# Optimization experiments

Hardware: AMD Instinct MI355X
Metric: run time of the kernel (lower is better)

## Reference

```python
import jax, jax.numpy as jnp
import numpy as np

HEADS = 16
DIM_HEAD = 64
MAX_FREQ = 256.0  # lucidrains RotaryEmbedding(freqs_for='pixel', max_freq=256)


def axial_freqs(H, W, dim_head):
    # per-axis rotary dim = dim_head // 2 (RotaryEmbedding(dim=head_dim//2))
    d = dim_head // 2
    base = jnp.linspace(1.0, MAX_FREQ / 2.0, d // 2) * jnp.pi  # (d/2,)

    def axis(n):
        pos = jnp.linspace(-1.0, 1.0, n)              # pixel positions
        f = pos[:, None] * base                        # (n, d/2)
        return jnp.repeat(f, 2, axis=-1)               # (n, d) interleaved pairs

    fh = jnp.broadcast_to(axis(H)[:, None, :], (H, W, d))
    fw = jnp.broadcast_to(axis(W)[None, :, :], (H, W, d))
    return jnp.concatenate([fh, fw], axis=-1)          # (H, W, dim_head)


def apply_rope(t, freqs):
    # t: (B,T,H,W,h,d); freqs: (H,W,d)
    f = freqs[:, :, None, :]                           # broadcast over heads
    x = t.reshape(t.shape[:-1] + (t.shape[-1] // 2, 2))
    x1, x2 = x[..., 0], x[..., 1]
    rot = jnp.stack([-x2, x1], axis=-1).reshape(t.shape)  # rotate_half (interleaved)
    return t * jnp.cos(f) + rot * jnp.sin(f)


def setup_inputs() -> dict:
    key = jax.random.key(0)
    k1, k2, k3 = jax.random.split(key, 3)
    B, T, H, W, D = 1, 8, 32, 32, 1024
    inner = HEADS * DIM_HEAD
    x = jax.random.normal(k1, (B, T, H, W, D), dtype=jnp.float32)
    Wqkv = jax.random.normal(k2, (D, 3 * inner), dtype=jnp.float32) * 0.02
    Wout = jax.random.normal(k3, (inner, D), dtype=jnp.float32) * 0.02
    bout = jnp.zeros((D,), dtype=jnp.float32)
    return {"x": x, "Wqkv": Wqkv, "Wout": Wout, "bout": bout}


def reference(x, Wqkv, Wout, bout):
    B, T, H, W, D = x.shape
    qkv = x @ Wqkv                                     # (B,T,H,W,3*inner)
    q, k, v = jnp.split(qkv, 3, axis=-1)
    shp = (B, T, H, W, HEADS, DIM_HEAD)
    q, k, v = q.reshape(shp), k.reshape(shp), v.reshape(shp)
    freqs = axial_freqs(H, W, DIM_HEAD)
    q = apply_rope(q, freqs)
    k = apply_rope(k, freqs)
    S = H * W
    q = q.reshape(B * T, S, HEADS, DIM_HEAD)
    k = k.reshape(B * T, S, HEADS, DIM_HEAD)
    v = v.reshape(B * T, S, HEADS, DIM_HEAD)
    scale = 1.0 / np.sqrt(DIM_HEAD).astype(np.float32)
    att = jnp.einsum('bshd,bthd->bhst', q, k) * scale  # (BT, h, S, S)
    att = jax.nn.softmax(att, axis=-1)
    o = jnp.einsum('bhst,bthd->bshd', att, v)          # (BT, S, h, d)
    o = o.reshape(B, T, H, W, HEADS * DIM_HEAD)
    return o @ Wout + bout
```

## Files before the change

### kernel.cpp

```cpp
#include <hip/hip_runtime.h>
#include <math.h>

#define DMODEL 1024
#define NQKV   3072
#define SEQ    1024
#define NH     16
#define DH     64
#define HS     (SEQ*DH)
constexpr float PI_F   = 3.14159265358979323846f;
constexpr float LOG2E  = 1.44269504088896f;

typedef _Float16 half8   __attribute__((ext_vector_type(8)));
typedef _Float16 half4   __attribute__((ext_vector_type(4)));
typedef float    floatx4 __attribute__((ext_vector_type(4)));

__device__ __forceinline__ void gload_lds16(const _Float16* g, _Float16* l) {
    __builtin_amdgcn_global_load_lds(
        (const __attribute__((address_space(1))) unsigned int*)g,
        (__attribute__((address_space(3)))       unsigned int*)l,
        16, 0, 0);
}

__global__ __launch_bounds__(256) void cvt_f16(
    const float* __restrict__ in, _Float16* __restrict__ out, int n)
{
    int i = (blockIdx.x*256 + threadIdx.x)*8;
    if (i >= n) return;
    float4 a = *(const float4*)(in + i);
    float4 b = *(const float4*)(in + i + 4);
    half8 h;
    h[0]=(_Float16)a.x; h[1]=(_Float16)a.y; h[2]=(_Float16)a.z; h[3]=(_Float16)a.w;
    h[4]=(_Float16)b.x; h[5]=(_Float16)b.y; h[6]=(_Float16)b.z; h[7]=(_Float16)b.w;
    *(half8*)(out + i) = h;
}

__global__ __launch_bounds__(256) void tr_cvt(
    const float* __restrict__ in, _Float16* __restrict__ out, int R, int C)
{
    __shared__ float T[32][33];
    const int bx = blockIdx.x, by = blockIdx.y;
    const int tx = threadIdx.x & 31, ty = threadIdx.x >> 5;
#pragma unroll
    for (int i = 0; i < 4; ++i)
        T[ty + i*8][tx] = in[(size_t)(by*32 + ty + i*8)*C + bx*32 + tx];
    __syncthreads();
#pragma unroll
    for (int i = 0; i < 4; ++i)
        out[(size_t)(bx*32 + ty + i*8)*R + by*32 + tx] = (_Float16)T[tx][ty + i*8];
}

__global__ __launch_bounds__(256) void gemm1_f16(
    const _Float16* __restrict__ A, const _Float16* __restrict__ Bt,
    _Float16* __restrict__ C, int M, int N, int K)
{
    __shared__ _Float16 As[128*32];
    __shared__ _Float16 Bs[128*32];
    const int tid = threadIdx.x;
    const int w = tid >> 6, lane = tid & 63, quad = lane >> 4, l = lane & 15;
    const int wm = (w & 1)*64, wn = (w >> 1)*64;
    const int m0 = blockIdx.y*128, n0 = blockIdx.x*128;

    const _Float16* a0 = A  + (size_t)(m0 + w*32      + (lane>>2))*K + (lane&3)*8;
    const _Float16* a1 = A  + (size_t)(m0 + w*32 + 16 + (lane>>2))*K + (lane&3)*8;
    const _Float16* b0 = Bt + (size_t)(n0 + w*32      + (lane>>2))*K + (lane&3)*8;
    const _Float16* b1 = Bt + (size_t)(n0 + w*32 + 16 + (lane>>2))*K + (lane&3)*8;
    _Float16* lA0 = As + w*1024;
    _Float16* lA1 = As + w*1024 + 512;
    _Float16* lB0 = Bs + w*1024;
    _Float16* lB1 = Bs + w*1024 + 512;

    floatx4 acc[4][4];
#pragma unroll
    for (int i = 0; i < 4; ++i)
#pragma unroll
        for (int j = 0; j < 4; ++j)
#pragma unroll
            for (int r = 0; r < 4; ++r) acc[i][j][r] = 0.f;

    for (int k0 = 0; k0 < K; k0 += 32) {
        __syncthreads();
        gload_lds16(a0, lA0); gload_lds16(a1, lA1);
        gload_lds16(b0, lB0); gload_lds16(b1, lB1);
        a0 += 32; a1 += 32; b0 += 32; b1 += 32;
        __syncthreads();
        half8 bf[4];
#pragma unroll
        for (int nt = 0; nt < 4; ++nt)
            bf[nt] = *(half8*)&Bs[(wn + nt*16 + l)*32 + quad*8];
#pragma unroll
        for (int mt = 0; mt < 4; ++mt) {
            half8 af = *(half8*)&As[(wm + mt*16 + l)*32 + quad*8];
#pragma unroll
            for (int nt = 0; nt < 4; ++nt)
                acc[mt][nt] = __builtin_amdgcn_mfma_f32_16x16x32_f16(af, bf[nt], acc[mt][nt], 0, 0, 0);
        }
    }
#pragma unroll
    for (int mt = 0; mt < 4; ++mt)
#pragma unroll
        for (int r = 0; r < 4; ++r) {
            size_t row = m0 + wm + mt*16 + quad*4 + r;
#pragma unroll
            for (int nt = 0; nt < 4; ++nt)
                C[row*N + n0 + wn + nt*16 + l] = (_Float16)acc[mt][nt][r];
        }
}

__global__ __launch_bounds__(256) void gemm2_f16(
    const _Float16* __restrict__ A, const _Float16* __restrict__ Bt,
    const float* __restrict__ bias, float* __restrict__ C, int M, int N, int K)
{
    __shared__ _Float16 As[128*32];
    __shared__ _Float16 Bs[128*32];
    const int tid = threadIdx.x;
    const int w = tid >> 6, lane = tid & 63, quad = lane >> 4, l = lane & 15;
    const int wm = (w & 1)*64, wn = (w >> 1)*64;
    const int m0 = blockIdx.y*128, n0 = blockIdx.x*128;

    const _Float16* a0 = A  + (size_t)(m0 + w*32      + (lane>>2))*K + (lane&3)*8;
    const _Float16* a1 = A  + (size_t)(m0 + w*32 + 16 + (lane>>2))*K + (lane&3)*8;
    const _Float16* b0 = Bt + (size_t)(n0 + w*32      + (lane>>2))*K + (lane&3)*8;
    const _Float16* b1 = Bt + (size_t)(n0 + w*32 + 16 + (lane>>2))*K + (lane&3)*8;
    _Float16* lA0 = As + w*1024;
    _Float16* lA1 = As + w*1024 + 512;
    _Float16* lB0 = Bs + w*1024;
    _Float16* lB1 = Bs + w*1024 + 512;

    floatx4 acc[4][4];
#pragma unroll
    for (int i = 0; i < 4; ++i)
#pragma unroll
        for (int j = 0; j < 4; ++j)
#pragma unroll
            for (int r = 0; r < 4; ++r) acc[i][j][r] = 0.f;

    for (int k0 = 0; k0 < K; k0 += 32) {
        __syncthreads();
        gload_lds16(a0, lA0); gload_lds16(a1, lA1);
        gload_lds16(b0, lB0); gload_lds16(b1, lB1);
        a0 += 32; a1 += 32; b0 += 32; b1 += 32;
        __syncthreads();
        half8 bf[4];
#pragma unroll
        for (int nt = 0; nt < 4; ++nt)
            bf[nt] = *(half8*)&Bs[(wn + nt*16 + l)*32 + quad*8];
#pragma unroll
        for (int mt = 0; mt < 4; ++mt) {
            half8 af = *(half8*)&As[(wm + mt*16 + l)*32 + quad*8];
#pragma unroll
            for (int nt = 0; nt < 4; ++nt)
                acc[mt][nt] = __builtin_amdgcn_mfma_f32_16x16x32_f16(af, bf[nt], acc[mt][nt], 0, 0, 0);
        }
    }
#pragma unroll
    for (int mt = 0; mt < 4; ++mt)
#pragma unroll
        for (int r = 0; r < 4; ++r) {
            size_t row = m0 + wm + mt*16 + quad*4 + r;
#pragma unroll
            for (int nt = 0; nt < 4; ++nt) {
                int col = n0 + wn + nt*16 + l;
                C[row*N + col] = acc[mt][nt][r] + bias[col];
            }
        }
}

__global__ __launch_bounds__(256) void rope_scatter(
    const _Float16* __restrict__ qkv,
    _Float16* __restrict__ qw, _Float16* __restrict__ kw,
    _Float16* __restrict__ vt)
{
    const int sc = blockIdx.x;
    const int bh = blockIdx.y;
    const int bt = bh >> 4, head = bh & 15;
    const int s0 = sc*64;
    const int tid = threadIdx.x;
    const int d0 = (tid & 7)*8;

    __shared__ _Float16 T[64][80];

#pragma unroll
    for (int half = 0; half < 2; ++half) {
        const int r = (tid >> 3) + half*32;
        const int s = s0 + r;
        const _Float16* src = qkv + (size_t)(bt*SEQ + s)*NQKV + head*DH + d0;
        half8 hq = *(const half8*)(src);
        half8 hk = *(const half8*)(src + DMODEL);
        half8 hv = *(const half8*)(src + 2*DMODEL);
        float fq[8], fk[8];
#pragma unroll
        for (int j = 0; j < 8; ++j) { fq[j] = (float)hq[j]; fk[j] = (float)hk[j]; }
        const int hp = s >> 5, wp = s & 31;
        const float ph = -1.0f + hp*(2.0f/31.0f);
        const float pw = -1.0f + wp*(2.0f/31.0f);
#pragma unroll
        for (int p = 0; p < 4; ++p) {
            int pg = (d0 >> 1) + p;
            float pos = (pg < 16) ? ph : pw;
            int   gi  = (pg < 16) ? pg : (pg - 16);
            float th  = pos * ((1.0f + gi*(127.0f/15.0f)) * PI_F);
            float sn, cs;
            sincosf(th, &sn, &cs);
            float q1 = fq[2*p], q2 = fq[2*p+1];
            fq[2*p]   = q1*cs - q2*sn;
            fq[2*p+1] = q2*cs + q1*sn;
            float k1 = fk[2*p], k2 = fk[2*p+1];
            fk[2*p]   = k1*cs - k2*sn;
            fk[2*p+1] = k2*cs + k1*sn;
        }
        half8 oq, ok;
        const float qsc = 0.125f * LOG2E;
#pragma unroll
        for (int j = 0; j < 8; ++j) {
            oq[j] = (_Float16)(fq[j]*qsc);
            ok[j] = (_Float16)fk[j];
        }
        *(half8*)(qw + (size_t)bh*HS + (size_t)s*DH + d0) = oq;
        *(half8*)(kw + (size_t)bh*HS + (size_t)s*DH + d0) = ok;
#pragma unroll
        for (int j = 0; j < 8; ++j) T[d0 + j][r] = hv[j];
    }
    __syncthreads();
    const int d = tid >> 2, so = (tid & 3)*16;
    half8 v0 = *(half8*)&T[d][so];
    half8 v1 = *(half8*)&T[d][so + 8];
    _Float16* dst = vt + (size_t)bh*HS + (size_t)d*SEQ + s0 + so;
    *(half8*)dst       = v0;
    *(half8*)(dst + 8) = v1;
}

#define BC  64
#define LDH 68

__global__ __launch_bounds__(256) void attn_mfma(
    const _Float16* __restrict__ qw, const _Float16* __restrict__ kw,
    const _Float16* __restrict__ vt, _Float16* __restrict__ om)
{
    const int qc = blockIdx.x;
    const int bh = blockIdx.y;
    const int tid  = threadIdx.x;
    const int w    = tid >> 6;
    const int lane = tid & 63;
    const int quad = lane >> 4;
    const int l    = lane & 15;

    __shared__ _Float16 Ks[2][BC][LDH];
    __shared__ _Float16 Vs[2][DH][LDH];
    __shared__ _Float16 Ps[4][32][LDH];
    __shared__ float    Ls[4][32];

    const _Float16* qp = qw + (size_t)bh*HS + (size_t)(qc*128 + w*32)*DH;
    const _Float16* kp = kw + (size_t)bh*HS;
    const _Float16* vp = vt + (size_t)bh*HS;

    half8 qf[2][2];
#pragma unroll
    for (int qt = 0; qt < 2; ++qt) {
        qf[qt][0] = *(const half8*)(qp + (size_t)(qt*16 + l)*DH + quad*8);
        qf[qt][1] = *(const half8*)(qp + (size_t)(qt*16 + l)*DH + quad*8 + 32);
    }

    const int rs = tid >> 3;
    const int cs = (tid & 7)*8;

    half8 kr0 = *(const half8*)(kp + (size_t)rs*DH + cs);
    half8 kr1 = *(const half8*)(kp + (size_t)(rs+32)*DH + cs);
    half8 vr0 = *(const half8*)(vp + (size_t)rs*SEQ + cs);
    half8 vr1 = *(const half8*)(vp + (size_t)(rs+32)*SEQ + cs);
    *(half8*)&Ks[0][rs][cs]    = kr0;
    *(half8*)&Ks[0][rs+32][cs] = kr1;
    *(half8*)&Vs[0][rs][cs]    = vr0;
    *(half8*)&Vs[0][rs+32][cs] = vr1;

    floatx4 Of[2][4];
#pragma unroll
    for (int qt = 0; qt < 2; ++qt)
#pragma unroll
        for (int dt = 0; dt < 4; ++dt)
#pragma unroll
            for (int r = 0; r < 4; ++r) Of[qt][dt][r] = 0.f;
    float lsum[2] = {0.f, 0.f};

    __syncthreads();

    for (int kc = 0; kc < SEQ/BC; ++kc) {
        const int cur = kc & 1;
        if (kc < SEQ/BC - 1) {
            const _Float16* kn = kp + (size_t)(kc+1)*BC*DH;
            const _Float16* vn = vp + (size_t)(kc+1)*BC;
            kr0 = *(const half8*)(kn + (size_t)rs*DH + cs);
            kr1 = *(const half8*)(kn + (size_t)(rs+32)*DH + cs);
            vr0 = *(const half8*)(vn + (size_t)rs*SEQ + cs);
            vr1 = *(const half8*)(vn + (size_t)(rs+32)*SEQ + cs);
        }

        floatx4 Sf[2][4];
#pragma unroll
        for (int kg = 0; kg < 4; ++kg) {
            half8 af0 = *(half8*)&Ks[cur][kg*16 + l][quad*8];
            half8 af1 = *(half8*)&Ks[cur][kg*16 + l][quad*8 + 32];
#pragma unroll
            for (int qt = 0; qt < 2; ++qt) {
                floatx4 a;
#pragma unroll
                for (int r = 0; r < 4; ++r) a[r] = 0.f;
                a = __builtin_amdgcn_mfma_f32_16x16x32_f16(af0, qf[qt][0], a, 0, 0, 0);
                a = __builtin_amdgcn_mfma_f32_16x16x32_f16(af1, qf[qt][1], a, 0, 0, 0);
                Sf[qt][kg] = a;
            }
        }
#pragma unroll
        for (int qt = 0; qt < 2; ++qt)
#pragma unroll
            for (int kg = 0; kg < 4; ++kg) {
                half4 p4;
#pragma unroll
                for (int r = 0; r < 4; ++r) {
                    float p = __builtin_amdgcn_exp2f(Sf[qt][kg][r]);
                    lsum[qt] += p;
                    p4[r] = (_Float16)p;
                }
                *(half4*)&Ps[w][qt*16 + l][kg*16 + quad*4] = p4;
            }
        half8 pa[2][2];
#pragma unroll
        for (int qt = 0; qt < 2; ++qt) {
            pa[qt][0] = *(half8*)&Ps[w][qt*16 + l][quad*8];
            pa[qt][1] = *(half8*)&Ps[w][qt*16 + l][quad*8 + 32];
        }
#pragma unroll
        for (int dt = 0; dt < 4; ++dt) {
            half8 vb0 = *(half8*)&Vs[cur][dt*16 + l][quad*8];
            half8 vb1 = *(half8*)&Vs[cur][dt*16 + l][quad*8 + 32];
#pragma unroll
            for (int qt = 0; qt < 2; ++qt) {
                Of[qt][dt] = __builtin_amdgcn_mfma_f32_16x16x32_f16(pa[qt][0], vb0, Of[qt][dt], 0, 0, 0);
                Of[qt][dt] = __builtin_amdgcn_mfma_f32_16x16x32_f16(pa[qt][1], vb1, Of[qt][dt], 0, 0, 0);
            }
        }

        if (kc < SEQ/BC - 1) {
            *(half8*)&Ks[1-cur][rs][cs]    = kr0;
            *(half8*)&Ks[1-cur][rs+32][cs] = kr1;
            *(half8*)&Vs[1-cur][rs][cs]    = vr0;
            *(half8*)&Vs[1-cur][rs+32][cs] = vr1;
        }
        __syncthreads();
    }

#pragma unroll
    for (int qt = 0; qt < 2; ++qt) {
        lsum[qt] += __shfl_xor(lsum[qt], 16);
        lsum[qt] += __shfl_xor(lsum[qt], 32);
        if (quad == 0) Ls[w][qt*16 + l] = lsum[qt];
    }
    const int bt = bh >> 4, head = bh & 15;
    _Float16* opf = om + (size_t)(bt*SEQ + qc*128 + w*32)*DMODEL + head*DH;
#pragma unroll
    for (int qt = 0; qt < 2; ++qt) {
        float inv[4];
#pragma unroll
        for (int r = 0; r < 4; ++r) inv[r] = 1.0f / Ls[w][qt*16 + quad*4 + r];
#pragma unroll
        for (int dt = 0; dt < 4; ++dt)
#pragma unroll
            for (int r = 0; r < 4; ++r)
                opf[(size_t)(qt*16 + quad*4 + r)*DMODEL + dt*16 + l] =
                    (_Float16)(Of[qt][dt][r]*inv[r]);
    }
}

extern "C" void kernel_launch(void* const* d_in, const int* in_sizes, int n_in,
                              void* d_out, int out_size, void* d_ws, size_t ws_size,
                              hipStream_t stream)
{
    const float* x    = (const float*)d_in[0];
    const float* Wqkv = (const float*)d_in[1];
    const float* Wout = (const float*)d_in[2];
    const float* bout = (const float*)d_in[3];
    float* out = (float*)d_out;

    _Float16* ws   = (_Float16*)d_ws;
    _Float16* Xh   = ws;
    _Float16* Wqkt = ws + 8388608;
    _Float16* Wot  = ws + 11534336;
    _Float16* qkvt = ws + 12582912;
    _Float16* qw   = ws + 37748736;
    _Float16* kw   = ws + 46137344;
    _Float16* vt   = ws + 54525952;
    _Float16* om   = qkvt;

    hipLaunchKernelGGL(cvt_f16, dim3(4096), dim3(256), 0, stream,
                       x, Xh, 8388608);
    hipLaunchKernelGGL(tr_cvt, dim3(96, 32), dim3(256), 0, stream,
                       Wqkv, Wqkt, 1024, 3072);
    hipLaunchKernelGGL(tr_cvt, dim3(32, 32), dim3(256), 0, stream,
                       Wout, Wot, 1024, 1024);
    hipLaunchKernelGGL(gemm1_f16, dim3(24, 64), dim3(256), 0, stream,
                       Xh, Wqkt, qkvt, 8192, NQKV, DMODEL);
    hipLaunchKernelGGL(rope_scatter, dim3(16, 128), dim3(256), 0, stream,
                       qkvt, qw, kw, vt);
    hipLaunchKernelGGL(attn_mfma, dim3(8, 128), dim3(256), 0, stream,
                       qw, kw, vt, om);
    hipLaunchKernelGGL(gemm2_f16, dim3(8, 64), dim3(256), 0, stream,
                       om, Wot, bout, out, 8192, DMODEL, DMODEL);
}
```

Baseline: 270.8 us.

## Fuse RoPE into QKV GEMM epilogue and merge prep conversion kernels

The QKV GEMM epilogue now applies axial RoPE and the softmax scale directly from accumulators, using lane shuffles for pair partners, and writes head-major q/k/v. This removes the intermediate fp16 qkv buffer and its full read in rope_scatter. V still needs a separate small transpose kernel. The three input conversion launches are also merged into one prep kernel to cut launch overhead. The trade-off is that epilogue stores become scattered 2-byte writes and sincos is computed per accumulator element.

After: 659.4 us. 144% more time.

```diff
diff --git a/kernel.cpp b/kernel.cpp
--- a/kernel.cpp
+++ b/kernel.cpp
@@ -21,24 +21,30 @@
         16, 0, 0);
 }
 
-__global__ __launch_bounds__(256) void cvt_f16(
-    const float* __restrict__ in, _Float16* __restrict__ out, int n)
-{
-    int i = (blockIdx.x*256 + threadIdx.x)*8;
-    if (i >= n) return;
-    float4 a = *(const float4*)(in + i);
-    float4 b = *(const float4*)(in + i + 4);
-    half8 h;
-    h[0]=(_Float16)a.x; h[1]=(_Float16)a.y; h[2]=(_Float16)a.z; h[3]=(_Float16)a.w;
-    h[4]=(_Float16)b.x; h[5]=(_Float16)b.y; h[6]=(_Float16)b.z; h[7]=(_Float16)b.w;
-    *(half8*)(out + i) = h;
-}
-
-__global__ __launch_bounds__(256) void tr_cvt(
-    const float* __restrict__ in, _Float16* __restrict__ out, int R, int C)
+__global__ __launch_bounds__(256) void prep(
+    const float* __restrict__ x, const float* __restrict__ Wqkv,
+    const float* __restrict__ Wout,
+    _Float16* __restrict__ Xh, _Float16* __restrict__ Wqkt,
+    _Float16* __restrict__ Wot)
 {
     __shared__ float T[32][33];
-    const int bx = blockIdx.x, by = blockIdx.y;
+    const int b = blockIdx.x;
+    if (b < 4096) {
+        int i = (b*256 + (int)threadIdx.x)*8;
+        float4 a0 = *(const float4*)(x + i);
+        float4 a1 = *(const float4*)(x + i + 4);
+        half8 h;
+        h[0]=(_Float16)a0.x; h[1]=(_Float16)a0.y; h[2]=(_Float16)a0.z; h[3]=(_Float16)a0.w;
+        h[4]=(_Float16)a1.x; h[5]=(_Float16)a1.y; h[6]=(_Float16)a1.z; h[7]=(_Float16)a1.w;
+        *(half8*)(Xh + i) = h;
+        return;
+    }
+    const float* in; _Float16* out; int C, bx, by;
+    if (b < 4096 + 3072) {
+        int bb = b - 4096; in = Wqkv; out = Wqkt; C = 3072; bx = bb % 96; by = bb / 96;
+    } else {
+        int bb = b - 7168; in = Wout; out = Wot;  C = 1024; bx = bb & 31; by = bb >> 5;
+    }
     const int tx = threadIdx.x & 31, ty = threadIdx.x >> 5;
 #pragma unroll
     for (int i = 0; i < 4; ++i)
@@ -46,24 +52,26 @@
     __syncthreads();
 #pragma unroll
     for (int i = 0; i < 4; ++i)
-        out[(size_t)(bx*32 + ty + i*8)*R + by*32 + tx] = (_Float16)T[tx][ty + i*8];
-}
-
-__global__ __launch_bounds__(256) void gemm1_f16(
+        out[(size_t)(bx*32 + ty + i*8)*1024 + by*32 + tx] = (_Float16)T[tx][ty + i*8];
+}
+
+__global__ __launch_bounds__(256) void gemm1_qkv(
     const _Float16* __restrict__ A, const _Float16* __restrict__ Bt,
-    _Float16* __restrict__ C, int M, int N, int K)
+    _Float16* __restrict__ qw, _Float16* __restrict__ kw,
+    _Float16* __restrict__ vrow)
 {
     __shared__ _Float16 As[128*32];
     __shared__ _Float16 Bs[128*32];
+    const int bx = blockIdx.x;
     const int tid = threadIdx.x;
     const int w = tid >> 6, lane = tid & 63, quad = lane >> 4, l = lane & 15;
     const int wm = (w & 1)*64, wn = (w >> 1)*64;
-    const int m0 = blockIdx.y*128, n0 = blockIdx.x*128;
-
-    const _Float16* a0 = A  + (size_t)(m0 + w*32      + (lane>>2))*K + (lane&3)*8;
-    const _Float16* a1 = A  + (size_t)(m0 + w*32 + 16 + (lane>>2))*K + (lane&3)*8;
-    const _Float16* b0 = Bt + (size_t)(n0 + w*32      + (lane>>2))*K + (lane&3)*8;
-    const _Float16* b1 = Bt + (size_t)(n0 + w*32 + 16 + (lane>>2))*K + (lane&3)*8;
+    const int m0 = blockIdx.y*128, n0 = bx*128;
+
+    const _Float16* a0 = A  + (size_t)(m0 + w*32      + (lane>>2))*DMODEL + (lane&3)*8;
+    const _Float16* a1 = A  + (size_t)(m0 + w*32 + 16 + (lane>>2))*DMODEL + (lane&3)*8;
+    const _Float16* b0 = Bt + (size_t)(n0 + w*32      + (lane>>2))*DMODEL + (lane&3)*8;
+    const _Float16* b1 = Bt + (size_t)(n0 + w*32 + 16 + (lane>>2))*DMODEL + (lane&3)*8;
     _Float16* lA0 = As + w*1024;
     _Float16* lA1 = As + w*1024 + 512;
     _Float16* lB0 = Bs + w*1024;
@@ -77,7 +85,7 @@
 #pragma unroll
             for (int r = 0; r < 4; ++r) acc[i][j][r] = 0.f;
 
-    for (int k0 = 0; k0 < K; k0 += 32) {
+    for (int k0 = 0; k0 < DMODEL; k0 += 32) {
         __syncthreads();
         gload_lds16(a0, lA0); gload_lds16(a1, lA1);
         gload_lds16(b0, lB0); gload_lds16(b1, lB1);
@@ -95,138 +103,71 @@
                 acc[mt][nt] = __builtin_amdgcn_mfma_f32_16x16x32_f16(af, bf[nt], acc[mt][nt], 0, 0, 0);
         }
     }
-#pragma unroll
-    for (int mt = 0; mt < 4; ++mt)
-#pragma unroll
-        for (int r = 0; r < 4; ++r) {
-            size_t row = m0 + wm + mt*16 + quad*4 + r;
-#pragma unroll
-            for (int nt = 0; nt < 4; ++nt)
-                C[row*N + n0 + wn + nt*16 + l] = (_Float16)acc[mt][nt][r];
-        }
-}
-
-__global__ __launch_bounds__(256) void gemm2_f16(
-    const _Float16* __restrict__ A, const _Float16* __restrict__ Bt,
-    const float* __restrict__ bias, float* __restrict__ C, int M, int N, int K)
-{
-    __shared__ _Float16 As[128*32];
-    __shared__ _Float16 Bs[128*32];
-    const int tid = threadIdx.x;
-    const int w = tid >> 6, lane = tid & 63, quad = lane >> 4, l = lane & 15;
-    const int wm = (w & 1)*64, wn = (w >> 1)*64;
-    const int m0 = blockIdx.y*128, n0 = blockIdx.x*128;
-
-    const _Float16* a0 = A  + (size_t)(m0 + w*32      + (lane>>2))*K + (lane&3)*8;
-    const _Float16* a1 = A  + (size_t)(m0 + w*32 + 16 + (lane>>2))*K + (lane&3)*8;
-    const _Float16* b0 = Bt + (size_t)(n0 + w*32      + (lane>>2))*K + (lane&3)*8;
-    const _Float16* b1 = Bt + (size_t)(n0 + w*32 + 16 + (lane>>2))*K + (lane&3)*8;
-    _Float16* lA0 = As + w*1024;
-    _Float16* lA1 = As + w*1024 + 512;
-    _Float16* lB0 = Bs + w*1024;
-    _Float16* lB1 = Bs + w*1024 + 512;
-
-    floatx4 acc[4][4];
-#pragma unroll
-    for (int i = 0; i < 4; ++i)
-#pragma unroll
-        for (int j = 0; j < 4; ++j)
-#pragma unroll
-            for (int r = 0; r < 4; ++r) acc[i][j][r] = 0.f;
-
-    for (int k0 = 0; k0 < K; k0 += 32) {
-        __syncthreads();
-        gload_lds16(a0, lA0); gload_lds16(a1, lA1);
-        gload_lds16(b0, lB0); gload_lds16(b1, lB1);
-        a0 += 32; a1 += 32; b0 += 32; b1 += 32;
-        __syncthreads();
-        half8 bf[4];
-#pragma unroll
-        for (int nt = 0; nt < 4; ++nt)
-            bf[nt] = *(half8*)&Bs[(wn + nt*16 + l)*32 + quad*8];
-#pragma unroll
-        for (int mt = 0; mt < 4; ++mt) {
-            half8 af = *(half8*)&As[(wm + mt*16 + l)*32 + quad*8];
-#pragma unroll
-            for (int nt = 0; nt < 4; ++nt)
-                acc[mt][nt] = __builtin_amdgcn_mfma_f32_16x16x32_f16(af, bf[nt], acc[mt][nt], 0, 0, 0);
-        }
-    }
-#pragma unroll
-    for (int mt = 0; mt < 4; ++mt)
-#pragma unroll
-        for (int r = 0; r < 4; ++r) {
-            size_t row = m0 + wm + mt*16 + quad*4 + r;
-#pragma unroll
-            for (int nt = 0; nt < 4; ++nt) {
-                int col = n0 + wn + nt*16 + l;
-                C[row*N + col] = acc[mt][nt][r] + bias[col];
-            }
-        }
-}
-
-__global__ __launch_bounds__(256) void rope_scatter(
-    const _Float16* __restrict__ qkv,
-    _Float16* __restrict__ qw, _Float16* __restrict__ kw,
-    _Float16* __restrict__ vt)
-{
-    const int sc = blockIdx.x;
+
+    const int t    = bx >> 3;
+    const int head = ((n0 + wn) >> 6) & 15;
+    const int bt   = m0 >> 10;
+    const int sbase = (m0 & 1023) + wm;
+    _Float16* obase = ((t == 0) ? qw : (t == 1) ? kw : vrow)
+                      + (size_t)(bt*NH + head)*HS;
+    if (t < 2) {
+        const float osc = (t == 0) ? 0.125f*LOG2E : 1.0f;
+        float bgi[4];
+#pragma unroll
+        for (int nt = 0; nt < 4; ++nt) {
+            int pg = nt*8 + (l >> 1);
+            int gi = (pg < 16) ? pg : pg - 16;
+            bgi[nt] = (1.0f + gi*(127.0f/15.0f))*PI_F;
+        }
+#pragma unroll
+        for (int mt = 0; mt < 4; ++mt)
+#pragma unroll
+            for (int r = 0; r < 4; ++r) {
+                int s  = sbase + mt*16 + quad*4 + r;
+                int hp = s >> 5, wp = s & 31;
+                float ph = -1.0f + hp*(2.0f/31.0f);
+                float pw = -1.0f + wp*(2.0f/31.0f);
+#pragma unroll
+                for (int nt = 0; nt < 4; ++nt) {
+                    float v  = acc[mt][nt][r];
+                    float v2 = __shfl_xor(v, 1);
+                    float pos = (nt < 2) ? ph : pw;
+                    float sn, cs;
+                    sincosf(pos*bgi[nt], &sn, &cs);
+                    float o = (l & 1) ? (v*cs + v2*sn) : (v*cs - v2*sn);
+                    obase[(size_t)s*DH + nt*16 + l] = (_Float16)(o*osc);
+                }
+            }
+    } else {
+#pragma unroll
+        for (int mt = 0; mt < 4; ++mt)
+#pragma unroll
+            for (int r = 0; r < 4; ++r) {
+                int s = sbase + mt*16 + quad*4 + r;
+#pragma unroll
+                for (int nt = 0; nt < 4; ++nt)
+                    obase[(size_t)s*DH + nt*16 + l] = (_Float16)acc[mt][nt][r];
+            }
+    }
+}
+
+__global__ __launch_bounds__(256) void v_tr(
+    const _Float16* __restrict__ vrow, _Float16* __restrict__ vt)
+{
+    __shared__ unsigned short T[32][33];
     const int bh = blockIdx.y;
-    const int bt = bh >> 4, head = bh & 15;
-    const int s0 = sc*64;
-    const int tid = threadIdx.x;
-    const int d0 = (tid & 7)*8;
-
-    __shared__ _Float16 T[64][80];
-
-#pragma unroll
-    for (int half = 0; half < 2; ++half) {
-        const int r = (tid >> 3) + half*32;
-        const int s = s0 + r;
-        const _Float16* src = qkv + (size_t)(bt*SEQ + s)*NQKV + head*DH + d0;
-        half8 hq = *(const half8*)(src);
-        half8 hk = *(const half8*)(src + DMODEL);
-        half8 hv = *(const half8*)(src + 2*DMODEL);
-        float fq[8], fk[8];
-#pragma unroll
-        for (int j = 0; j < 8; ++j) { fq[j] = (float)hq[j]; fk[j] = (float)hk[j]; }
-        const int hp = s >> 5, wp = s & 31;
-        const float ph = -1.0f + hp*(2.0f/31.0f);
-        const float pw = -1.0f + wp*(2.0f/31.0f);
-#pragma unroll
-        for (int p = 0; p < 4; ++p) {
-            int pg = (d0 >> 1) + p;
-            float pos = (pg < 16) ? ph : pw;
-            int   gi  = (pg < 16) ? pg : (pg - 16);
-            float th  = pos * ((1.0f + gi*(127.0f/15.0f)) * PI_F);
-            float sn, cs;
-            sincosf(th, &sn, &cs);
-            float q1 = fq[2*p], q2 = fq[2*p+1];
-            fq[2*p]   = q1*cs - q2*sn;
-            fq[2*p+1] = q2*cs + q1*sn;
-            float k1 = fk[2*p], k2 = fk[2*p+1];
-            fk[2*p]   = k1*cs - k2*sn;
-            fk[2*p+1] = k2*cs + k1*sn;
-        }
-        half8 oq, ok;
-        const float qsc = 0.125f * LOG2E;
-#pragma unroll
-        for (int j = 0; j < 8; ++j) {
-            oq[j] = (_Float16)(fq[j]*qsc);
-            ok[j] = (_Float16)fk[j];
-        }
-        *(half8*)(qw + (size_t)bh*HS + (size_t)s*DH + d0) = oq;
-        *(half8*)(kw + (size_t)bh*HS + (size_t)s*DH + d0) = ok;
-#pragma unroll
-        for (int j = 0; j < 8; ++j) T[d0 + j][r] = hv[j];
-    }
+    const int td = blockIdx.x & 1;
+    const int ts = blockIdx.x >> 1;
+    const int tx = threadIdx.x & 31, ty = threadIdx.x >> 5;
+    const unsigned short* src = (const unsigned short*)(vrow + (size_t)bh*HS);
+    unsigned short*       dst = (unsigned short*)(vt + (size_t)bh*HS);
+#pragma unroll
+    for (int i = 0; i < 4; ++i)
+        T[ty + i*8][tx] = src[(size_t)(ts*32 + ty + i*8)*DH + td*32 + tx];
     __syncthreads();
-    const int d = tid >> 2, so = (tid & 3)*16;
-    half8 v0 = *(half8*)&T[d][so];
-    half8 v1 = *(half8*)&T[d][so + 8];
-    _Float16* dst = vt + (size_t)bh*HS + (size_t)d*SEQ + s0 + so;
-    *(half8*)dst       = v0;
-    *(half8*)(dst + 8) = v1;
+#pragma unroll
+    for (int i = 0; i < 4; ++i)
+        dst[(size_t)(td*32 + ty + i*8)*SEQ + ts*32 + tx] = T[tx][ty + i*8];
 }
 
 #define BC  64
@@ -370,6 +311,65 @@
     }
 }
 
+__global__ __launch_bounds__(256) void gemm2_f16(
+    const _Float16* __restrict__ A, const _Float16* __restrict__ Bt,
+    const float* __restrict__ bias, float* __restrict__ C, int M, int N, int K)
+{
+    __shared__ _Float16 As[128*32];
+    __shared__ _Float16 Bs[128*32];
+    const int tid = threadIdx.x;
+    const int w = tid >> 6, lane = tid & 63, quad = lane >> 4, l = lane & 15;
+    const int wm = (w & 1)*64, wn = (w >> 1)*64;
+    const int m0 = blockIdx.y*128, n0 = blockIdx.x*128;
+
+    const _Float16* a0 = A  + (size_t)(m0 + w*32      + (lane>>2))*K + (lane&3)*8;
+    const _Float16* a1 = A  + (size_t)(m0 + w*32 + 16 + (lane>>2))*K + (lane&3)*8;
+    const _Float16* b0 = Bt + (size_t)(n0 + w*32      + (lane>>2))*K + (lane&3)*8;
+    const _Float16* b1 = Bt + (size_t)(n0 + w*32 + 16 + (lane>>2))*K + (lane&3)*8;
+    _Float16* lA0 = As + w*1024;
+    _Float16* lA1 = As + w*1024 + 512;
+    _Float16* lB0 = Bs + w*1024;
+    _Float16* lB1 = Bs + w*1024 + 512;
+
+    floatx4 acc[4][4];
+#pragma unroll
+    for (int i = 0; i < 4; ++i)
+#pragma unroll
+        for (int j = 0; j < 4; ++j)
+#pragma unroll
+            for (int r = 0; r < 4; ++r) acc[i][j][r] = 0.f;
+
+    for (int k0 = 0; k0 < K; k0 += 32) {
+        __syncthreads();
+        gload_lds16(a0, lA0); gload_lds16(a1, lA1);
+        gload_lds16(b0, lB0); gload_lds16(b1, lB1);
+        a0 += 32; a1 += 32; b0 += 32; b1 += 32;
+        __syncthreads();
+        half8 bf[4];
+#pragma unroll
+        for (int nt = 0; nt < 4; ++nt)
+            bf[nt] = *(half8*)&Bs[(wn + nt*16 + l)*32 + quad*8];
+#pragma unroll
+        for (int mt = 0; mt < 4; ++mt) {
+            half8 af = *(half8*)&As[(wm + mt*16 + l)*32 + quad*8];
+#pragma unroll
+            for (int nt = 0; nt < 4; ++nt)
+                acc[mt][nt] = __builtin_amdgcn_mfma_f32_16x16x32_f16(af, bf[nt], acc[mt][nt], 0, 0, 0);
+        }
+    }
+#pragma unroll
+    for (int mt = 0; mt < 4; ++mt)
+#pragma unroll
+        for (int r = 0; r < 4; ++r) {
+            size_t row = m0 + wm + mt*16 + quad*4 + r;
+#pragma unroll
+            for (int nt = 0; nt < 4; ++nt) {
+                int col = n0 + wn + nt*16 + l;
+                C[row*N + col] = acc[mt][nt][r] + bias[col];
+            }
+        }
+}
+
 extern "C" void kernel_launch(void* const* d_in, const int* in_sizes, int n_in,
                               void* d_out, int out_size, void* d_ws, size_t ws_size,
                               hipStream_t stream)
@@ -384,22 +384,18 @@
     _Float16* Xh   = ws;
     _Float16* Wqkt = ws + 8388608;
     _Float16* Wot  = ws + 11534336;
-    _Float16* qkvt = ws + 12582912;
-    _Float16* qw   = ws + 37748736;
-    _Float16* kw   = ws + 46137344;
-    _Float16* vt   = ws + 54525952;
-    _Float16* om   = qkvt;
-
-    hipLaunchKernelGGL(cvt_f16, dim3(4096), dim3(256), 0, stream,
-                       x, Xh, 8388608);
-    hipLaunchKernelGGL(tr_cvt, dim3(96, 32), dim3(256), 0, stream,
-                       Wqkv, Wqkt, 1024, 3072);
-    hipLaunchKernelGGL(tr_cvt, dim3(32, 32), dim3(256), 0, stream,
-                       Wout, Wot, 1024, 1024);
-    hipLaunchKernelGGL(gemm1_f16, dim3(24, 64), dim3(256), 0, stream,
-                       Xh, Wqkt, qkvt, 8192, NQKV, DMODEL);
-    hipLaunchKernelGGL(rope_scatter, dim3(16, 128), dim3(256), 0, stream,
-                       qkvt, qw, kw, vt);
+    _Float16* qw   = ws + 12582912;
+    _Float16* kw   = ws + 20971520;
+    _Float16* vrow = ws + 29360128;
+    _Float16* vt   = ws + 37748736;
+    _Float16* om   = ws + 46137344;
+
+    hipLaunchKernelGGL(prep, dim3(8192), dim3(256), 0, stream,
+                       x, Wqkv, Wout, Xh, Wqkt, Wot);
+    hipLaunchKernelGGL(gemm1_qkv, dim3(24, 64), dim3(256), 0, stream,
+                       Xh, Wqkt, qw, kw, vrow);
+    hipLaunchKernelGGL(v_tr, dim3(64, 128), dim3(256), 0, stream,
+                       vrow, vt);
     hipLaunchKernelGGL(attn_mfma, dim3(8, 128), dim3(256), 0, stream,
                        qw, kw, vt, om);
     hipLaunchKernelGGL(gemm2_f16, dim3(8, 64), dim3(256), 0, stream,
```
